# Optimization experiments

Hardware: AMD Instinct MI355X
Metric: run time of the kernel (lower is better)

## Reference

```python
import jax, jax.numpy as jnp
import numpy as np

B, C_LOCAL, C_GUIDE, C2, H, W = 16, 256, 256, 256, 64, 64
MID = C2 // 2          # mlp hidden channels
CQ = C_LOCAL // 4      # offset_gen hidden channels (also = groups)
EPS = 1e-5             # BatchNorm eps (inference mode)


def _conv(x, w, pad=0, groups=1, b=None):
    out = jax.lax.conv_general_dilated(
        x, w, window_strides=(1, 1), padding=((pad, pad), (pad, pad)),
        dimension_numbers=('NCHW', 'OIHW', 'NCHW'), feature_group_count=groups)
    if b is not None:
        out = out + b[None, :, None, None]
    return out


def _bn(x, g, b, m, v):
    scale = g / jnp.sqrt(v + EPS)
    return x * scale[None, :, None, None] + (b - m * scale)[None, :, None, None]


def _grid_sample(img, grid):
    # img: [C,H,W]; grid: [H,W,2] with (x,y) in [-1,1]; bilinear, zeros padding,
    # align_corners=False (pixel = ((g+1)*size - 1)/2)
    C, Hh, Ww = img.shape
    ix = (grid[..., 0] + 1.0) * (Ww * 0.5) - 0.5
    iy = (grid[..., 1] + 1.0) * (Hh * 0.5) - 0.5
    x0 = jnp.floor(ix); y0 = jnp.floor(iy)
    x1 = x0 + 1.0;      y1 = y0 + 1.0
    wx1 = ix - x0; wx0 = 1.0 - wx1
    wy1 = iy - y0; wy0 = 1.0 - wy1

    def gather(xi, yi):
        valid = (xi >= 0) & (xi < Ww) & (yi >= 0) & (yi < Hh)
        xc = jnp.clip(xi, 0, Ww - 1).astype(jnp.int32)
        yc = jnp.clip(yi, 0, Hh - 1).astype(jnp.int32)
        return img[:, yc, xc] * valid.astype(img.dtype)[None]  # [C,H,W]

    return (gather(x0, y0) * (wx0 * wy0)[None]
            + gather(x1, y0) * (wx1 * wy0)[None]
            + gather(x0, y1) * (wx0 * wy1)[None]
            + gather(x1, y1) * (wx1 * wy1)[None])


def setup_inputs() -> dict:
    key = jax.random.key(0)
    ks = jax.random.split(key, 20)
    w = lambda k, s: jax.random.normal(k, s, jnp.float32) * 0.05
    return {
        'x_local': jax.random.normal(ks[0], (B, C_LOCAL, H, W), jnp.float32),
        'x_guide': jax.random.normal(ks[1], (B, C_GUIDE, H, W), jnp.float32),
        'w_align': w(ks[2], (C2, C_GUIDE, 1, 1)),
        'bn1_g': 1.0 + 0.1 * jax.random.normal(ks[3], (C2,), jnp.float32),
        'bn1_b': 0.1 * jax.random.normal(ks[4], (C2,), jnp.float32),
        'bn1_m': 0.1 * jax.random.normal(ks[5], (C2,), jnp.float32),
        'bn1_v': 0.5 + jax.random.uniform(ks[6], (C2,), jnp.float32),
        'w_off1': w(ks[7], (CQ, 4, 3, 3)),   # grouped: in-ch per group = C_LOCAL/CQ = 4
        'w_off2': w(ks[8], (2, CQ, 1, 1)),
        'b_off2': 0.1 * jax.random.normal(ks[9], (2,), jnp.float32),
        'w_mlp1': w(ks[10], (MID, C_LOCAL, 1, 1)),
        'bn2_g': 1.0 + 0.1 * jax.random.normal(ks[11], (MID,), jnp.float32),
        'bn2_b': 0.1 * jax.random.normal(ks[12], (MID,), jnp.float32),
        'bn2_m': 0.1 * jax.random.normal(ks[13], (MID,), jnp.float32),
        'bn2_v': 0.5 + jax.random.uniform(ks[14], (MID,), jnp.float32),
        'w_mlp2': w(ks[15], (C2, MID, 1, 1)),
    }


def reference(x_local, x_guide, w_align, bn1_g, bn1_b, bn1_m, bn1_v,
              w_off1, w_off2, b_off2, w_mlp1, bn2_g, bn2_b, bn2_m, bn2_v,
              w_mlp2):
    # align(x_guide): 1x1 conv + BN
    g = _bn(_conv(x_guide, w_align), bn1_g, bn1_b, bn1_m, bn1_v)
    # offset_gen(x_local): grouped 3x3 conv -> SiLU -> 1x1 conv (bias) -> [B,2,H,W]
    off = _conv(x_local, w_off1, pad=1, groups=CQ)
    off = _conv(jax.nn.silu(off), w_off2, b=b_off2)
    # base grid in [-1,1], (x,y) last
    ys = jnp.linspace(-1.0, 1.0, H)
    xs = jnp.linspace(-1.0, 1.0, W)
    gy, gx = jnp.meshgrid(ys, xs, indexing='ij')
    base = jnp.stack((gx, gy), axis=-1)                      # [H,W,2]
    v_grid = base[None] + off.transpose(0, 2, 3, 1) * (2.0 / max(H, W))
    g_aligned = jax.vmap(_grid_sample)(g, v_grid)            # [B,C2,H,W]
    # mlp(x_local): 1x1 conv -> BN -> GELU(exact) -> 1x1 conv
    l = _conv(x_local, w_mlp1)
    l = jax.nn.gelu(_bn(l, bn2_g, bn2_b, bn2_m, bn2_v), approximate=False)
    l = _conv(l, w_mlp2)
    return jax.nn.silu(g_aligned + l)
```

## Files before the change

kernel.cpp:

```cpp
#include <hip/hip_runtime.h>

typedef unsigned short u16;
typedef __bf16 bf16x8 __attribute__((ext_vector_type(8)));
typedef float f32x4 __attribute__((ext_vector_type(4)));
typedef u16 u16x2 __attribute__((ext_vector_type(2)));
typedef u16 u16x4 __attribute__((ext_vector_type(4)));
typedef u16 u16x8 __attribute__((ext_vector_type(8)));

#define EPS 1e-5f

__device__ __forceinline__ u16 f2bf(float f) {
  unsigned u = __builtin_bit_cast(unsigned, f);
  u += 0x7FFFu + ((u >> 16) & 1u);
  return (u16)(u >> 16);
}
__device__ __forceinline__ float bf2f(u16 h) {
  unsigned u = ((unsigned)h) << 16;
  return __builtin_bit_cast(float, u);
}

__global__ void prep_weights(
    const float* __restrict__ wa, const float* __restrict__ g1, const float* __restrict__ b1,
    const float* __restrict__ m1, const float* __restrict__ v1,
    const float* __restrict__ w1, const float* __restrict__ g2, const float* __restrict__ b2,
    const float* __restrict__ m2, const float* __restrict__ v2,
    const float* __restrict__ w2,
    u16* __restrict__ Acat, u16* __restrict__ w1_o,
    float* __restrict__ bias1, float* __restrict__ bias2) {
  int c = blockIdx.x, k = threadIdx.x;
  float s1 = g1[c] / sqrtf(v1[c] + EPS);
  if (k < 256) Acat[c * 384 + k] = f2bf(wa[c * 256 + k] * s1);
  else         Acat[c * 384 + k] = f2bf(w2[c * 128 + (k - 256)]);
  if (c < 128) {
    float s2 = g2[c] / sqrtf(v2[c] + EPS);
    if (k < 256) w1_o[c * 256 + k] = f2bf(w1[c * 256 + k] * s2);
    if (k == 256) bias2[c] = b2[c] - m2[c] * s2;
  }
  if (k == 0) bias1[c] = b1[c] - m1[c] * s1;
}

__global__ __launch_bounds__(256) void gconv_kernel(
    const float* __restrict__ xl, const float* __restrict__ w1,
    u16* __restrict__ sbuf) {
  __shared__ float tile[4][18][66];
  const int tid = threadIdx.x;
  const int band = blockIdx.x;
  const int q = blockIdx.y;
  const int b = blockIdx.z;
  const float* xb = xl + ((size_t)b * 256 + 4 * q) * 4096;
  for (int i = tid; i < 4 * 18 * 66; i += 256) {
    int ci = i / (18 * 66);
    int rem = i - ci * (18 * 66);
    int r = rem / 66, c = rem - r * 66;
    int gy = band * 16 - 1 + r, gx = c - 1;
    float v = 0.f;
    if ((unsigned)gy < 64u && (unsigned)gx < 64u)
      v = xb[(size_t)ci * 4096 + gy * 64 + gx];
    tile[ci][r][c] = v;
  }
  float wq[36];
#pragma unroll
  for (int i = 0; i < 36; ++i) wq[i] = w1[q * 36 + i];
  __syncthreads();
  const int c = tid & 63, r0 = tid >> 6;
  u16* sp = sbuf + ((size_t)(b * 64 + q)) * 4096 + band * 1024;
#pragma unroll
  for (int k = 0; k < 4; ++k) {
    int r = r0 * 4 + k;
    float s = 0.f;
#pragma unroll
    for (int ci = 0; ci < 4; ++ci)
#pragma unroll
      for (int dy = 0; dy < 3; ++dy)
#pragma unroll
        for (int dx = 0; dx < 3; ++dx)
          s += wq[ci * 9 + dy * 3 + dx] * tile[ci][r + dy][c + dx];
    sp[r * 64 + c] = f2bf(s / (1.f + __expf(-s)));
  }
}

__global__ __launch_bounds__(256) void sampler_kernel(
    const u16* __restrict__ sbuf, const float* __restrict__ w2,
    const float* __restrict__ b2, const float* __restrict__ xg,
    u16* __restrict__ xgs, float* __restrict__ wsum) {
  __shared__ float sw2[128];
  __shared__ float part[2][4][64];
  const int wg = blockIdx.x;
  const int idx = (wg & 7) * 128 + (wg >> 3);
  const int b = idx >> 6, row = idx & 63;
  const int tid = threadIdx.x, px = tid & 63, ko = tid >> 6;
  if (tid < 128) sw2[tid] = w2[tid];
  __syncthreads();
  const u16* sp = sbuf + (size_t)b * 64 * 4096 + row * 64 + px;
  float ax = 0.f, ay = 0.f;
#pragma unroll
  for (int qq = 0; qq < 16; ++qq) {
    int q = ko * 16 + qq;
    float v = bf2f(sp[(size_t)q * 4096]);
    ax += sw2[q] * v;
    ay += sw2[64 + q] * v;
  }
  part[0][ko][px] = ax;
  part[1][ko][px] = ay;
  __syncthreads();
  float ox = part[0][0][px] + part[0][1][px] + part[0][2][px] + part[0][3][px] + b2[0];
  float oy = part[1][0][px] + part[1][1][px] + part[1][2][px] + part[1][3][px] + b2[1];
  float ix = (64.f / 63.f) * (float)px + ox - 0.5f;
  float iy = (64.f / 63.f) * (float)row + oy - 0.5f;
  float x0f = floorf(ix), y0f = floorf(iy);
  int x0 = (int)x0f, y0 = (int)y0f;
  float wx1 = ix - x0f, wx0 = 1.f - wx1;
  float wy1 = iy - y0f, wy0 = 1.f - wy1;
  bool vx0 = (unsigned)x0 < 64u, vx1 = (unsigned)(x0 + 1) < 64u;
  bool vy0 = (unsigned)y0 < 64u, vy1 = (unsigned)(y0 + 1) < 64u;
  int x0c = min(max(x0, 0), 63), x1c = min(max(x0 + 1, 0), 63);
  int y0c = min(max(y0, 0), 63), y1c = min(max(y0 + 1, 0), 63);
  float w00 = (vx0 && vy0) ? wx0 * wy0 : 0.f;
  float w10 = (vx1 && vy0) ? wx1 * wy0 : 0.f;
  float w01 = (vx0 && vy1) ? wx0 * wy1 : 0.f;
  float w11 = (vx1 && vy1) ? wx1 * wy1 : 0.f;
  const int p = row * 64 + px;
  if (ko == 0) wsum[(size_t)b * 4096 + p] = w00 + w10 + w01 + w11;
  const int i00 = y0c * 64 + x0c, i10 = y0c * 64 + x1c;
  const int i01 = y1c * 64 + x0c, i11 = y1c * 64 + x1c;
  const float* xb = xg + (size_t)b * 256 * 4096;
  u16* xo = xgs + (size_t)b * 256 * 4096 + p;
#pragma unroll 4
  for (int k = ko; k < 256; k += 4) {
    const float* bb = xb + (size_t)k * 4096;
    float v = w00 * bb[i00] + w10 * bb[i10] + w01 * bb[i01] + w11 * bb[i11];
    xo[(size_t)k * 4096] = f2bf(v);
  }
}

__global__ __launch_bounds__(256, 2) void gemm_h(
    const u16* __restrict__ A, const float* __restrict__ Bsrc,
    u16* __restrict__ Out, const float* __restrict__ bias) {
  __shared__ u16 Al[128][40];
  __shared__ u16 Bl[128][40];
  const int tid = threadIdx.x;
  const int b = blockIdx.y;
  const int n0 = blockIdx.x * 128;
  const int wave = tid >> 6, lane = tid & 63;
  const int wr = wave >> 1, wc = wave & 1;
  const int lr = lane & 15, kg = lane >> 4;
  f32x4 acc[4][4] = {};
  const float* Bf = Bsrc + (size_t)b * 256 * 4096;

  for (int kt = 0; kt < 8; ++kt) {
    {
      int m = tid >> 1, pos = (tid & 1) * 16;
      u16x8 v0 = *(const u16x8*)(A + (size_t)m * 256 + kt * 32 + pos);
      u16x8 v1 = *(const u16x8*)(A + (size_t)m * 256 + kt * 32 + pos + 8);
      *(u16x8*)&Al[m][pos] = v0;
      *(u16x8*)&Al[m][pos + 8] = v1;
    }
    {
      int nq = tid & 31, kq = tid >> 5;
      int kb = kt * 32 + kq * 4;
      int nb = n0 + nq * 4;
      f32x4 r[4];
#pragma unroll
      for (int i = 0; i < 4; ++i)
        r[i] = *(const f32x4*)(Bf + (size_t)(kb + i) * 4096 + nb);
#pragma unroll
      for (int j = 0; j < 4; ++j) {
        u16x4 w = {f2bf(r[0][j]), f2bf(r[1][j]), f2bf(r[2][j]), f2bf(r[3][j])};
        *(u16x4*)&Bl[nq * 4 + j][kq * 4] = w;
      }
    }
    __syncthreads();
    bf16x8 af[4], bfr[4];
#pragma unroll
    for (int i = 0; i < 4; ++i) {
      af[i] = *(const bf16x8*)&Al[wr * 64 + i * 16 + lr][kg * 8];
      bfr[i] = *(const bf16x8*)&Bl[wc * 64 + i * 16 + lr][kg * 8];
    }
#pragma unroll
    for (int i = 0; i < 4; ++i)
#pragma unroll
      for (int j = 0; j < 4; ++j)
        acc[i][j] = __builtin_amdgcn_mfma_f32_16x16x32_bf16(af[i], bfr[j], acc[i][j], 0, 0, 0);
    __syncthreads();
  }
  u16* O = Out + (size_t)b * 4096 * 128;
#pragma unroll
  for (int i = 0; i < 4; ++i) {
    int rb = wr * 64 + i * 16 + kg * 4;
    f32x4 b4 = *(const f32x4*)(bias + rb);
#pragma unroll
    for (int j = 0; j < 4; ++j) {
      int col = n0 + wc * 64 + j * 16 + lr;
      u16x4 w;
#pragma unroll
      for (int e = 0; e < 4; ++e) {
        float v = acc[i][j][e] + b4[e];
        v = 0.5f * v * (1.f + erff(v * 0.70710678118f));
        w[e] = f2bf(v);
      }
      *(u16x4*)(O + (size_t)col * 128 + rb) = w;
    }
  }
}

__global__ __launch_bounds__(512, 2) void gemm_final(
    const u16* __restrict__ A,
    const u16* __restrict__ xgs,
    const u16* __restrict__ hb,
    const float* __restrict__ bias1, const float* __restrict__ wsum,
    float* __restrict__ out) {
  __shared__ u16 Al[256][40];
  __shared__ u16 Bl[128][40];
  const int tid = threadIdx.x;
  const int b = blockIdx.y;
  const int n0 = blockIdx.x * 128;
  const int wave = tid >> 6, lane = tid & 63;
  const int wr = wave >> 1, wc = wave & 1;
  const int lr = lane & 15, kg = lane >> 4;
  f32x4 acc[4][4] = {};
  const u16* xb = xgs + (size_t)b * 256 * 4096;
  const u16* hp = hb + (size_t)b * 4096 * 128;

  for (int kt = 0; kt < 12; ++kt) {
#pragma unroll
    for (int c = 0; c < 2; ++c) {
      int ch = tid + c * 512;
      int m = ch >> 2, pos = (ch & 3) * 8;
      *(u16x8*)&Al[m][pos] = *(const u16x8*)(A + (size_t)m * 384 + kt * 32 + pos);
    }
    if (kt < 8) {
      int kq2 = tid >> 5;
      int nq = tid & 31;
      int k0 = kt * 32 + kq2 * 2;
      u16x4 r0 = *(const u16x4*)(xb + (size_t)k0 * 4096 + n0 + nq * 4);
      u16x4 r1 = *(const u16x4*)(xb + (size_t)(k0 + 1) * 4096 + n0 + nq * 4);
#pragma unroll
      for (int j = 0; j < 4; ++j) {
        u16x2 w = {r0[j], r1[j]};
        *(u16x2*)&Bl[nq * 4 + j][kq2 * 2] = w;
      }
    } else {
      int pl = tid >> 2, kq = tid & 3;
      *(u16x8*)&Bl[pl][kq * 8] =
          *(const u16x8*)(hp + (size_t)(n0 + pl) * 128 + (kt - 8) * 32 + kq * 8);
    }
    __syncthreads();
    bf16x8 af[4], bfr[4];
#pragma unroll
    for (int i = 0; i < 4; ++i) {
      af[i] = *(const bf16x8*)&Al[wr * 64 + i * 16 + lr][kg * 8];
      bfr[i] = *(const bf16x8*)&Bl[wc * 64 + i * 16 + lr][kg * 8];
    }
#pragma unroll
    for (int i = 0; i < 4; ++i)
#pragma unroll
      for (int j = 0; j < 4; ++j)
        acc[i][j] = __builtin_amdgcn_mfma_f32_16x16x32_bf16(af[i], bfr[j], acc[i][j], 0, 0, 0);
    __syncthreads();
  }

  float* Ob = out + (size_t)b * 256 * 4096;
#pragma unroll
  for (int j = 0; j < 4; ++j) {
    int col = n0 + wc * 64 + j * 16 + lr;
    float ws = wsum[(size_t)b * 4096 + col];
#pragma unroll
    for (int i = 0; i < 4; ++i) {
      int rb = wr * 64 + i * 16 + kg * 4;
      f32x4 b4 = *(const f32x4*)(bias1 + rb);
#pragma unroll
      for (int e = 0; e < 4; ++e) {
        float v = acc[i][j][e] + b4[e] * ws;
        Ob[(size_t)(rb + e) * 4096 + col] = v / (1.f + __expf(-v));
      }
    }
  }
}

extern "C" void kernel_launch(void* const* d_in, const int* in_sizes, int n_in,
                              void* d_out, int out_size, void* d_ws, size_t ws_size,
                              hipStream_t stream) {
  const float* x_local = (const float*)d_in[0];
  const float* x_guide = (const float*)d_in[1];
  const float* w_align = (const float*)d_in[2];
  const float* bn1_g = (const float*)d_in[3];
  const float* bn1_b = (const float*)d_in[4];
  const float* bn1_m = (const float*)d_in[5];
  const float* bn1_v = (const float*)d_in[6];
  const float* w_off1 = (const float*)d_in[7];
  const float* w_off2 = (const float*)d_in[8];
  const float* b_off2 = (const float*)d_in[9];
  const float* w_mlp1 = (const float*)d_in[10];
  const float* bn2_g = (const float*)d_in[11];
  const float* bn2_b = (const float*)d_in[12];
  const float* bn2_m = (const float*)d_in[13];
  const float* bn2_v = (const float*)d_in[14];
  const float* w_mlp2 = (const float*)d_in[15];

  char* ws = (char*)d_ws;
  u16* Acat = (u16*)(ws + 0);
  u16* w1_bf = (u16*)(ws + 196608);
  float* bias1 = (float*)(ws + 262144);
  float* bias2 = (float*)(ws + 263168);
  float* wsum = (float*)(ws + 263680);
  u16* xgs = (u16*)(ws + 525824);
  u16* hbuf = (u16*)(ws + 34080256);
  u16* sbuf = hbuf;

  prep_weights<<<256, 384, 0, stream>>>(
      w_align, bn1_g, bn1_b, bn1_m, bn1_v,
      w_mlp1, bn2_g, bn2_b, bn2_m, bn2_v, w_mlp2,
      Acat, w1_bf, bias1, bias2);

  gconv_kernel<<<dim3(4, 64, 16), 256, 0, stream>>>(x_local, w_off1, sbuf);

  sampler_kernel<<<1024, 256, 0, stream>>>(sbuf, w_off2, b_off2, x_guide, xgs, wsum);

  gemm_h<<<dim3(32, 16), 256, 0, stream>>>(w1_bf, x_local, hbuf, bias2);

  gemm_final<<<dim3(32, 16), 512, 0, stream>>>(Acat, xgs, hbuf, bias1, wsum, (float*)d_out);
}
```

Baseline: 132.0 us.

## Split sampler into coordinate kernel and channel-parallel gather kernel

The offset projection and sampling-coordinate computation move into a separate coords_kernel that writes per-pixel (ix,iy) and the weight sum to a workspace buffer. The sampler then launches four times as many blocks, each handling 64 channels of one row, which raises parallelism for the gather over x_guide. In exchange there is an extra kernel launch and a small round-trip of the coords buffer, and the floor and weight maths is repeated in every sampler block.

Result: no change. 130.3 us (-1.3%).

```diff
diff --git a/kernel.cpp b/kernel.cpp
--- a/kernel.cpp
+++ b/kernel.cpp
@@ -79,34 +79,50 @@
   }
 }
 
-__global__ __launch_bounds__(256) void sampler_kernel(
+__global__ __launch_bounds__(256) void coords_kernel(
     const u16* __restrict__ sbuf, const float* __restrict__ w2,
-    const float* __restrict__ b2, const float* __restrict__ xg,
-    u16* __restrict__ xgs, float* __restrict__ wsum) {
+    const float* __restrict__ b2, float* __restrict__ coords,
+    float* __restrict__ wsum) {
   __shared__ float sw2[128];
-  __shared__ float part[2][4][64];
-  const int wg = blockIdx.x;
-  const int idx = (wg & 7) * 128 + (wg >> 3);
-  const int b = idx >> 6, row = idx & 63;
-  const int tid = threadIdx.x, px = tid & 63, ko = tid >> 6;
+  const int tid = threadIdx.x;
   if (tid < 128) sw2[tid] = w2[tid];
   __syncthreads();
-  const u16* sp = sbuf + (size_t)b * 64 * 4096 + row * 64 + px;
+  const int b = blockIdx.y;
+  const int p = blockIdx.x * 256 + tid;
+  const u16* sp = sbuf + (size_t)b * 64 * 4096 + p;
   float ax = 0.f, ay = 0.f;
-#pragma unroll
-  for (int qq = 0; qq < 16; ++qq) {
-    int q = ko * 16 + qq;
+#pragma unroll 8
+  for (int q = 0; q < 64; ++q) {
     float v = bf2f(sp[(size_t)q * 4096]);
     ax += sw2[q] * v;
     ay += sw2[64 + q] * v;
   }
-  part[0][ko][px] = ax;
-  part[1][ko][px] = ay;
-  __syncthreads();
-  float ox = part[0][0][px] + part[0][1][px] + part[0][2][px] + part[0][3][px] + b2[0];
-  float oy = part[1][0][px] + part[1][1][px] + part[1][2][px] + part[1][3][px] + b2[1];
-  float ix = (64.f / 63.f) * (float)px + ox - 0.5f;
-  float iy = (64.f / 63.f) * (float)row + oy - 0.5f;
+  int y = p >> 6, x = p & 63;
+  float ix = (64.f / 63.f) * (float)x + ax + b2[0] - 0.5f;
+  float iy = (64.f / 63.f) * (float)y + ay + b2[1] - 0.5f;
+  ((float2*)coords)[(size_t)b * 4096 + p] = make_float2(ix, iy);
+  float x0f = floorf(ix), y0f = floorf(iy);
+  int x0 = (int)x0f, y0 = (int)y0f;
+  float wx1 = ix - x0f, wx0 = 1.f - wx1;
+  float wy1 = iy - y0f, wy0 = 1.f - wy1;
+  bool vx0 = (unsigned)x0 < 64u, vx1 = (unsigned)(x0 + 1) < 64u;
+  bool vy0 = (unsigned)y0 < 64u, vy1 = (unsigned)(y0 + 1) < 64u;
+  float s = (vx0 && vy0 ? wx0 * wy0 : 0.f) + (vx1 && vy0 ? wx1 * wy0 : 0.f) +
+            (vx0 && vy1 ? wx0 * wy1 : 0.f) + (vx1 && vy1 ? wx1 * wy1 : 0.f);
+  wsum[(size_t)b * 4096 + p] = s;
+}
+
+__global__ __launch_bounds__(256) void sampler_kernel(
+    const float* __restrict__ xg, const float* __restrict__ coords,
+    u16* __restrict__ xgs) {
+  const int wg = blockIdx.x;
+  const int id = (wg & 7) * 512 + (wg >> 3);
+  const int kq = id >> 10;
+  const int b = (id >> 6) & 15, row = id & 63;
+  const int px = threadIdx.x & 63, ko = threadIdx.x >> 6;
+  const int p = row * 64 + px;
+  float2 cd = ((const float2*)coords)[(size_t)b * 4096 + p];
+  float ix = cd.x, iy = cd.y;
   float x0f = floorf(ix), y0f = floorf(iy);
   int x0 = (int)x0f, y0 = (int)y0f;
   float wx1 = ix - x0f, wx0 = 1.f - wx1;
@@ -119,17 +135,16 @@
   float w10 = (vx1 && vy0) ? wx1 * wy0 : 0.f;
   float w01 = (vx0 && vy1) ? wx0 * wy1 : 0.f;
   float w11 = (vx1 && vy1) ? wx1 * wy1 : 0.f;
-  const int p = row * 64 + px;
-  if (ko == 0) wsum[(size_t)b * 4096 + p] = w00 + w10 + w01 + w11;
   const int i00 = y0c * 64 + x0c, i10 = y0c * 64 + x1c;
   const int i01 = y1c * 64 + x0c, i11 = y1c * 64 + x1c;
-  const float* xb = xg + (size_t)b * 256 * 4096;
-  u16* xo = xgs + (size_t)b * 256 * 4096 + p;
-#pragma unroll 4
-  for (int k = ko; k < 256; k += 4) {
-    const float* bb = xb + (size_t)k * 4096;
-    float v = w00 * bb[i00] + w10 * bb[i10] + w01 * bb[i01] + w11 * bb[i11];
-    xo[(size_t)k * 4096] = f2bf(v);
+  const int k0 = kq * 64 + ko * 16;
+  const float* bb = xg + ((size_t)b * 256 + k0) * 4096;
+  u16* xo = xgs + ((size_t)b * 256 + k0) * 4096 + p;
+#pragma unroll
+  for (int kk = 0; kk < 16; ++kk) {
+    const float* bp = bb + (size_t)kk * 4096;
+    float v = w00 * bp[i00] + w10 * bp[i10] + w01 * bp[i01] + w11 * bp[i11];
+    xo[(size_t)kk * 4096] = f2bf(v);
   }
 }
 
@@ -303,8 +318,9 @@
   float* bias1 = (float*)(ws + 262144);
   float* bias2 = (float*)(ws + 263168);
   float* wsum = (float*)(ws + 263680);
-  u16* xgs = (u16*)(ws + 525824);
-  u16* hbuf = (u16*)(ws + 34080256);
+  float* coords = (float*)(ws + 525824);
+  u16* xgs = (u16*)(ws + 1050112);
+  u16* hbuf = (u16*)(ws + 34604544);
   u16* sbuf = hbuf;
 
   prep_weights<<<256, 384, 0, stream>>>(
@@ -314,7 +330,9 @@
 
   gconv_kernel<<<dim3(4, 64, 16), 256, 0, stream>>>(x_local, w_off1, sbuf);
 
-  sampler_kernel<<<1024, 256, 0, stream>>>(sbuf, w_off2, b_off2, x_guide, xgs, wsum);
+  coords_kernel<<<dim3(16, 16), 256, 0, stream>>>(sbuf, w_off2, b_off2, coords, wsum);
+
+  sampler_kernel<<<4096, 256, 0, stream>>>(x_guide, coords, xgs);
 
   gemm_h<<<dim3(32, 16), 256, 0, stream>>>(w1_bf, x_local, hbuf, bias2);
 
```
